# Kernel optimization log

Hardware: AMD Instinct MI355X
Metric: run time of the kernel (lower is better)

## Reference

```python
import math
import jax, jax.numpy as jnp
import numpy as np

N = 2048
HID = 1024
ALPHA = 0.5
BETA = 0.1  # greedy term is zero when coords is None


def setup_inputs() -> dict:
    key = jax.random.key(0)
    k1, k2, k3, k4 = jax.random.split(key, 4)
    node_emb = jax.random.normal(k1, (N, HID), jnp.float32)
    demands = jax.random.uniform(k2, (N,), jnp.float32)  # each < 1 << capacity
    # query_net: Linear(hid+2 -> hid); key_net: Linear(hid -> hid)
    Wq = jax.random.normal(k3, (HID, HID + 2), jnp.float32) / math.sqrt(HID + 2)
    bq = jnp.zeros((HID,), jnp.float32)
    Wk = jax.random.normal(k4, (HID, HID), jnp.float32) / math.sqrt(HID)
    bk = jnp.zeros((HID,), jnp.float32)
    return {"node_emb": node_emb, "demands": demands, "Wq": Wq, "bq": bq,
            "Wk": Wk, "bk": bk, "capacity": 40, "depot_idx": 0}


def _decode(node_emb, demands, Wq, bq, Wk, bk, capacity, depot_idx):
    n, h = node_emb.shape
    cap = jnp.float32(capacity)
    inv_sqrt = 1.0 / math.sqrt(h)
    # key_net is a per-node linear map: precompute once (same math as per-step gather+linear)
    K = node_emb @ Wk.T + bk  # [N, H]
    idx = jnp.arange(n)
    # demands < 1, capacity = 40 => >= 39 customers per route => few depot returns;
    # T = N + N//8 safely bounds customer picks + route-closing depot emissions.
    T = n + n // 8
    visited0 = jnp.zeros((n,), bool).at[depot_idx].set(True)

    def step(carry, _):
        visited, load, last, done = carry
        feasible = (~visited) & (demands <= load)
        has_cand = jnp.any(feasible)
        # context = [emb(last), load/capacity, avgd]; avgd = 0 since coords is None
        ctx = jnp.concatenate([node_emb[last],
                               jnp.stack([load / cap, jnp.float32(0.0)])])
        q = Wq @ ctx + bq                      # [H]
        s = ALPHA * ((K @ q) * inv_sqrt)       # [N] scores over all nodes
        s_m = jnp.where(feasible, s, -jnp.inf)
        cand = jnp.argmax(s_m)
        take = has_cand & (~done)
        nxt = jnp.where(take, cand, depot_idx).astype(jnp.int32)
        step_score = jnp.where(take, s[cand], jnp.float32(0.0))
        visited = visited | ((idx == cand) & take)
        load = jnp.where(take, load - demands[cand], cap)  # route end resets load
        done = done | ((~take) & jnp.all(visited))
        return (visited, load, nxt, done), (nxt, step_score)

    carry0 = (visited0, cap, jnp.int32(depot_idx), jnp.bool_(False))
    _, (seq, scores) = jax.lax.scan(step, carry0, None, length=T)
    tour = jnp.concatenate([jnp.array([depot_idx], seq.dtype), seq])  # [T+1]
    return tour, scores


def reference(node_emb, demands, Wq, bq, Wk, bk, capacity, depot_idx):
    # tour: flat visitation order; routes are the segments between depot occurrences
    # (trailing depots are padding once all customers are served).
    # scores: selected decoder score at each step (0 at depot/padding steps).
    return _decode(node_emb, demands, Wq, bq, Wk, bk, capacity, depot_idx)
```

## Files before the change

### kernel.cpp

```cpp
#include <hip/hip_runtime.h>
#include <hip/hip_bf16.h>


#define NN 2048
#define HH 1024
#define TSTEPS (NN + NN / 8)
#define TILE 64
#define KT 16
#define KCAND 128
#define KL 15

__global__ __launch_bounds__(256) void prep_wqh(const float* __restrict__ Wq,
                                                float* __restrict__ Wqh) {
  int id = blockIdx.x * 256 + threadIdx.x;
  int r = id >> 10, c = id & 1023;
  Wqh[id] = Wq[r * (HH + 2) + c];
}

__global__ __launch_bounds__(256) void gemm_nt(const float* __restrict__ A, int lda,
                                               const float* __restrict__ B, int ldb,
                                               float* __restrict__ C, int ldc,
                                               int K, const float* __restrict__ bias) {
  __shared__ float As[KT][TILE + 4];
  __shared__ float Bs[KT][TILE + 4];
  const int i0 = blockIdx.y * TILE;
  const int j0 = blockIdx.x * TILE;
  const int t = threadIdx.x;
  const int srow = t >> 2, sq = t & 3;
  const int tx = t & 15, ty = t >> 4;
  float acc[4][4] = {};
  for (int k0 = 0; k0 < K; k0 += KT) {
    float4 av = *(const float4*)&A[(size_t)(i0 + srow) * lda + k0 + sq * 4];
    float4 bv = *(const float4*)&B[(size_t)(j0 + srow) * ldb + k0 + sq * 4];
    __syncthreads();
    As[sq * 4 + 0][srow] = av.x; As[sq * 4 + 1][srow] = av.y;
    As[sq * 4 + 2][srow] = av.z; As[sq * 4 + 3][srow] = av.w;
    Bs[sq * 4 + 0][srow] = bv.x; Bs[sq * 4 + 1][srow] = bv.y;
    Bs[sq * 4 + 2][srow] = bv.z; Bs[sq * 4 + 3][srow] = bv.w;
    __syncthreads();
#pragma unroll
    for (int k = 0; k < KT; ++k) {
      float4 a4 = *(const float4*)&As[k][ty * 4];
      float4 b4 = *(const float4*)&Bs[k][tx * 4];
      float a[4] = {a4.x, a4.y, a4.z, a4.w};
      float b[4] = {b4.x, b4.y, b4.z, b4.w};
#pragma unroll
      for (int m = 0; m < 4; ++m)
#pragma unroll
        for (int n = 0; n < 4; ++n) acc[m][n] = fmaf(a[m], b[n], acc[m][n]);
    }
  }
  float bb[4] = {0.f, 0.f, 0.f, 0.f};
  if (bias) {
#pragma unroll
    for (int n = 0; n < 4; ++n) bb[n] = bias[j0 + tx * 4 + n];
  }
#pragma unroll
  for (int m = 0; m < 4; ++m) {
    float4 st = {acc[m][0] + bb[0], acc[m][1] + bb[1], acc[m][2] + bb[2], acc[m][3] + bb[3]};
    *(float4*)&C[(size_t)(i0 + ty * 4 + m) * ldc + j0 + tx * 4] = st;
  }
}

__global__ __launch_bounds__(64) void uv_k(const float* __restrict__ Kmat,
                                           const float* __restrict__ Wq,
                                           const float* __restrict__ bq,
                                           float* __restrict__ u, float* __restrict__ v) {
  int i = blockIdx.x;
  int lane = threadIdx.x;
  float su = 0.f, sv = 0.f;
#pragma unroll
  for (int m = 0; m < HH / 64; ++m) {
    int j = lane + 64 * m;
    float kv = Kmat[(size_t)i * HH + j];
    su = fmaf(kv, Wq[(size_t)j * (HH + 2) + HH], su);
    sv = fmaf(kv, bq[j], sv);
  }
#pragma unroll
  for (int off = 32; off; off >>= 1) {
    su += __shfl_down(su, off, 64);
    sv += __shfl_down(sv, off, 64);
  }
  if (lane == 0) { u[i] = su; v[i] = sv; }
}

__global__ __launch_bounds__(256) void umax_k(const float* __restrict__ u,
                                              float* __restrict__ umaxp) {
  __shared__ float sm[256];
  int t = threadIdx.x;
  float m = 0.f;
  for (int i = t; i < NN; i += 256) m = fmaxf(m, fabsf(u[i]));
  sm[t] = m;
  __syncthreads();
  for (int s = 128; s; s >>= 1) {
    if (t < s) sm[t] = fmaxf(sm[t], sm[t + s]);
    __syncthreads();
  }
  if (t == 0) *umaxp = sm[0];
}

__device__ __forceinline__ unsigned f2key(float f) {
  unsigned x = __float_as_uint(f);
  return x ^ ((x >> 31) ? 0xFFFFFFFFu : 0x80000000u);
}
__device__ __forceinline__ float key2f(unsigned k) {
  unsigned x = (k & 0x80000000u) ? (k ^ 0x80000000u) : ~k;
  return __uint_as_float(x);
}
__device__ __forceinline__ unsigned ub16(float x) {
  unsigned b = __float_as_uint(x);
  if (x > 0.f && (b & 0xFFFFu)) b += 0x10000u;
  return b >> 16;
}
__global__ __launch_bounds__(256) void prep_cand(const float* __restrict__ GT,
                                                 uint2* __restrict__ cand,
                                                 unsigned* __restrict__ pc16,
                                                 unsigned* __restrict__ thrpk) {
  __shared__ float rowv[NN];
  __shared__ int hist[256];
  __shared__ unsigned c128k[KCAND];
  __shared__ int c128i[KCAND];
  __shared__ int s_d, s_need, s_gt, s_eq, s_gt2, s_eq2, s_flag;
  const int row = blockIdx.x, t = threadIdx.x;
  for (int i = t; i < NN; i += 256) rowv[i] = GT[(size_t)row * NN + i];
  __syncthreads();
  unsigned prefix = 0;
  int need = KCAND;
  for (int pass = 0; pass < 4; ++pass) {
    hist[t] = 0;
    __syncthreads();
    const int shift = 24 - 8 * pass;
    for (int i = t; i < NN; i += 256) {
      unsigned k = f2key(rowv[i]);
      if (pass == 0 || (k >> (shift + 8)) == (prefix >> (shift + 8)))
        atomicAdd(&hist[(k >> shift) & 0xFF], 1);
    }
    __syncthreads();
    if (t == 0) {
      int cum = 0, d = 255;
      for (; d > 0; --d) {
        if (cum + hist[d] >= need) break;
        cum += hist[d];
      }
      s_d = d;
      s_need = need - cum;
    }
    __syncthreads();
    prefix |= ((unsigned)s_d) << shift;
    need = s_need;
    __syncthreads();
  }
  const unsigned thrk = prefix;
  if (t == 0) { s_gt = 0; s_eq = 0; }
  __syncthreads();
  for (int i = t; i < NN; i += 256) {
    unsigned k = f2key(rowv[i]);
    if (k > thrk) {
      int p = atomicAdd(&s_gt, 1);
      cand[(size_t)row * KCAND + p] = make_uint2(__float_as_uint(rowv[i]), (unsigned)i);
      c128k[p] = k;
      c128i[p] = i;
    }
  }
  __syncthreads();
  const int cgt = s_gt;
  for (int i = t; i < NN; i += 256) {
    if (f2key(rowv[i]) == thrk) {
      int p = atomicAdd(&s_eq, 1);
      if (p < KCAND - cgt) {
        cand[(size_t)row * KCAND + cgt + p] = make_uint2(__float_as_uint(rowv[i]), (unsigned)i);
        c128k[cgt + p] = thrk;
        c128i[cgt + p] = i;
      }
    }
  }
  __syncthreads();
  unsigned pfx2 = 0;
  need = KL;
  for (int pass = 0; pass < 4; ++pass) {
    hist[t] = 0;
    __syncthreads();
    const int shift = 24 - 8 * pass;
    for (int i = t; i < KCAND; i += 256) {
      unsigned k = c128k[i];
      if (pass == 0 || (k >> (shift + 8)) == (pfx2 >> (shift + 8)))
        atomicAdd(&hist[(k >> shift) & 0xFF], 1);
    }
    __syncthreads();
    if (t == 0) {
      int cum = 0, d = 255;
      for (; d > 0; --d) {
        if (cum + hist[d] >= need) break;
        cum += hist[d];
      }
      s_d = d;
      s_need = need - cum;
    }
    __syncthreads();
    pfx2 |= ((unsigned)s_d) << shift;
    need = s_need;
    __syncthreads();
  }
  const unsigned thrk15 = pfx2;
  if (t == 0) { s_gt2 = 0; s_eq2 = 0; s_flag = 0; }
  __syncthreads();
  for (int i = t; i < KCAND; i += 256) {
    if (c128k[i] > thrk15) {
      int p = atomicAdd(&s_gt2, 1);
      pc16[(size_t)row * KL + p] = (c128k[i] & 0xFFFFF800u) | (unsigned)c128i[i];
      if (fabsf(key2f(c128k[i])) >= 128.0f) s_flag = 1;
    }
  }
  __syncthreads();
  const int cgt2 = s_gt2;
  for (int i = t; i < KCAND; i += 256) {
    if (c128k[i] == thrk15) {
      int p = atomicAdd(&s_eq2, 1);
      if (p < KL - cgt2)
        pc16[(size_t)row * KL + cgt2 + p] = (thrk15 & 0xFFFFF800u) | (unsigned)c128i[i];
    }
  }
  if (t == 0 && fabsf(key2f(thrk15)) >= 128.0f) s_flag = 1;
  __syncthreads();
  if (t == 0) {
    float t15 = s_flag ? __builtin_inff() : key2f(thrk15);
    thrpk[row] = (ub16(t15) << 16) | ub16(key2f(thrk));
  }
}

__global__ __launch_bounds__(256) void warm_k(const float* __restrict__ a, int n,
                                              float* __restrict__ sink) {
  float s = 0.f;
  const float4* a4 = (const float4*)a;
  for (int i = threadIdx.x; i < n / 4; i += 256) {
    float4 x = a4[i];
    s += x.x + x.y + x.z + x.w;
  }
  if (s == 1.2345e-30f) sink[blockIdx.x] = s;
}

#define DPP_MERGE2(CTRL)                                                      \
  {                                                                           \
    int ovb = __builtin_amdgcn_update_dpp(                                    \
        (int)0xFF800000, __float_as_int(bv), (CTRL), 0xf, 0xf, false);        \
    int oib = __builtin_amdgcn_update_dpp(                                    \
        0x7fffffff, bi, (CTRL), 0xf, 0xf, false);                             \
    float ov = __int_as_float(ovb);                                           \
    if (ov > bv || (ov == bv && oib < bi)) { bv = ov; bi = oib; }             \
  }

#define DPP_TOP2(CTRL)                                                        \
  {                                                                           \
    int ovb = __builtin_amdgcn_update_dpp(                                    \
        (int)0xFF800000, __float_as_int(bv1), (CTRL), 0xf, 0xf, false);       \
    int oib = __builtin_amdgcn_update_dpp(                                    \
        0x7fffffff, bi1, (CTRL), 0xf, 0xf, false);                            \
    int ov2b = __builtin_amdgcn_update_dpp(                                   \
        (int)0xFF800000, __float_as_int(bv2), (CTRL), 0xf, 0xf, false);       \
    float ov1 = __int_as_float(ovb);                                          \
    float ov2 = __int_as_float(ov2b);                                         \
    float lose = fminf(bv1, ov1);                                             \
    if (ov1 > bv1 || (ov1 == bv1 && oib < bi1)) { bv1 = ov1; bi1 = oib; }     \
    bv2 = fmaxf(fmaxf(bv2, ov2), lose);                                       \
  }

__global__ __launch_bounds__(64, 1) void decode(const float* __restrict__ GT,
                                                const uint2* __restrict__ cand,
                                                const unsigned* __restrict__ pc16,
                                                const unsigned* __restrict__ thrpkg,
                                                const float* __restrict__ umaxp,
                                                const float* __restrict__ u,
                                                const float* __restrict__ demands,
                                                const int* __restrict__ capp,
                                                const int* __restrict__ depotp,
                                                float* __restrict__ out) {
  __shared__ __align__(16) unsigned s_pc[NN * KL + 64];
  __shared__ __align__(16) float2 s_du[NN];
  __shared__ __align__(16) unsigned s_thr[NN];
  __shared__ __align__(16) float s_lr[TSTEPS];
  __shared__ __align__(16) unsigned short s_tour[TSTEPS + 2];

  const int lane = threadIdx.x;
  const int depot = *depotp;
  const float capf = (float)(*capp);
  const float umaxv = *umaxp;
  const float INF = __builtin_inff();
  const float NEGINF = -INF;
  const float C0 = 0.015625f;
  const float MARGIN = 0.5f;
  const float EGM = 0.0625f;
  float* sduf = (float*)s_du;

  for (int i = lane; i < NN; i += 64) {
    s_du[i] = make_float2(demands[i], u[i]);
    s_thr[i] = thrpkg[i];
  }
  {
    const uint4* p4 = (const uint4*)pc16;
    uint4* q4 = (uint4*)s_pc;
    for (int i = lane; i < NN * KL / 4; i += 64) q4[i] = p4[i];
  }
  if (lane == 0) {
    sduf[2 * depot] = INF;
    s_tour[0] = (unsigned short)depot;
  }

  int done = 0, ntaken = 0, lasts = depot;
  float load = capf;
  float lr = load / capf;
  int step = 0;
  const int lcl = (lane < KL) ? lane : (KL - 1);

  for (; step < TSTEPS; ++step) {
    const int row = lasts;
    unsigned pw = s_pc[row * KL + lcl];
    unsigned pk = s_thr[row];
    int i1x = (int)(pw & 0x7FFu);
    float g1 = key2f(pw & 0xFFFFF800u);
    float2 du1 = s_du[i1x];
    float t1 = fmaf(du1.y, lr, g1);
    bool act = (lane < KL) && (du1.x <= load);
    float bv1 = act ? t1 : NEGINF;
    int bi1 = act ? i1x : 0x7fffffff;
    float bv2 = NEGINF;
    DPP_TOP2(0x111); DPP_TOP2(0x112); DPP_TOP2(0x114); DPP_TOP2(0x118);
    float rv1 = __int_as_float(__builtin_amdgcn_readlane(__float_as_int(bv1), 15));
    int ri1 = __builtin_amdgcn_readlane(bi1, 15);
    float rv2 = __int_as_float(__builtin_amdgcn_readlane(__float_as_int(bv2), 15));
    float thr1 = __uint_as_float(pk & 0xFFFF0000u);
    const float B1 = fmaf(lr, umaxv, thr1) + MARGIN;
    int take, nxt;
    if (rv1 > B1 && rv1 > rv2 + EGM) {
      take = 1; nxt = ri1;
    } else {
      uint4 cc = ((const uint4*)(cand + (size_t)row * KCAND))[lane];
      float bv = NEGINF;
      int bi = 0x7fffffff;
      {
        float ga = __uint_as_float(cc.x); int ia = (int)cc.y;
        float gb = __uint_as_float(cc.z); int ib = (int)cc.w;
        float2 da = s_du[ia];
        float2 db = s_du[ib];
        float ta = fmaf(da.y, lr, ga);
        float tb = fmaf(db.y, lr, gb);
        if ((da.x <= load) && (ta > bv || (ta == bv && ia < bi))) { bv = ta; bi = ia; }
        if ((db.x <= load) && (tb > bv || (tb == bv && ib < bi))) { bv = tb; bi = ib; }
      }
      DPP_MERGE2(0x111); DPP_MERGE2(0x112); DPP_MERGE2(0x114);
      DPP_MERGE2(0x118); DPP_MERGE2(0x142); DPP_MERGE2(0x143);
      float rbv = __int_as_float(__builtin_amdgcn_readlane(__float_as_int(bv), 63));
      int rbi = __builtin_amdgcn_readlane(bi, 63);
      float thr2 = __uint_as_float(pk << 16);
      const float B2 = fmaf(lr, umaxv, thr2) + MARGIN;
      if (rbv > B2) {
        take = 1; nxt = rbi;
      } else {
        const float4* rowp = (const float4*)(GT + (size_t)row * NN);
        const float4* du4 = (const float4*)s_du;
        float fv = NEGINF;
        int fi = NN;
#pragma unroll
        for (int r = 0; r < 8; ++r) {
          float4 g4 = rowp[r * 64 + lane];
          float4 pA = du4[(r * 64 + lane) * 2];
          float4 pB = du4[(r * 64 + lane) * 2 + 1];
          float gl[4] = {g4.x, g4.y, g4.z, g4.w};
          float dl[4] = {pA.x, pA.z, pB.x, pB.z};
          float ul[4] = {pA.y, pA.w, pB.y, pB.w};
          float cv = NEGINF;
          int cj = 0;
#pragma unroll
          for (int j = 0; j < 4; ++j) {
            float tt = fmaf(ul[j], lr, gl[j]);
            bool feas = (dl[j] <= load);
            if (feas && tt > cv) { cv = tt; cj = j; }
          }
          if (cv > fv) { fv = cv; fi = 4 * (r * 64 + lane) + cj; }
        }
        float bv = fv;
        int bi = fi;
        DPP_MERGE2(0x111); DPP_MERGE2(0x112); DPP_MERGE2(0x114);
        DPP_MERGE2(0x118); DPP_MERGE2(0x142); DPP_MERGE2(0x143);
        float fbv = __int_as_float(__builtin_amdgcn_readlane(__float_as_int(bv), 63));
        int fbi = __builtin_amdgcn_readlane(bi, 63);
        take = (fbv > NEGINF) ? 1 : 0;
        nxt = take ? fbi : depot;
      }
    }

    if (lane == 0) {
      s_tour[1 + step] = (unsigned short)nxt;
      s_lr[step] = take ? lr : -1.0f;
    }
    if (take) {
      float dwin = s_du[nxt].x;
      load = load - dwin;
      ntaken++;
      if (lane == 0) sduf[2 * nxt] = INF;
    } else {
      load = capf;
      if (ntaken == NN - 1) done = 1;
    }
    lasts = nxt;
    lr = load / capf;
    if (done) { ++step; break; }
  }

  for (int q = step + lane; q < TSTEPS; q += 64) {
    s_tour[1 + q] = (unsigned short)depot;
    s_lr[q] = -1.0f;
  }
  for (int i = lane; i <= TSTEPS; i += 64) out[i] = (float)s_tour[i];
  for (int s = lane; s < TSTEPS; s += 64) {
    float lrs = s_lr[s];
    float sc = 0.0f;
    if (lrs >= 0.0f) {
      int lastI = (int)s_tour[s];
      int biI = (int)s_tour[s + 1];
      float g = GT[(size_t)lastI * NN + biI];
      sc = fmaf(s_du[biI].y, lrs, g) * C0;
    }
    out[1 + TSTEPS + s] = sc;
  }
}

extern "C" void kernel_launch(void* const* d_in, const int* in_sizes, int n_in,
                              void* d_out, int out_size, void* d_ws, size_t ws_size,
                              hipStream_t stream) {
  const float* emb     = (const float*)d_in[0];
  const float* demands = (const float*)d_in[1];
  const float* Wq      = (const float*)d_in[2];
  const float* bq      = (const float*)d_in[3];
  const float* Wk      = (const float*)d_in[4];
  const float* bk      = (const float*)d_in[5];
  const int* cap       = (const int*)d_in[6];
  const int* depot     = (const int*)d_in[7];
  float* out           = (float*)d_out;

  char* ws = (char*)d_ws;
  float* Kmat = (float*)(ws);
  float* Z    = (float*)(ws + ((size_t)8 << 20));
  float* GT   = (float*)(ws + ((size_t)16 << 20));
  float* Wqh  = (float*)(ws + ((size_t)32 << 20));
  float* u    = (float*)(ws + ((size_t)36 << 20));
  float* v    = (float*)(ws + ((size_t)36 << 20) + 8192);
  unsigned* thrpkg = (unsigned*)(ws + ((size_t)36 << 20) + 16384);
  float* umax = (float*)(ws + ((size_t)36 << 20) + 24576);
  float* sink = (float*)(ws + ((size_t)36 << 20) + 32768);
  uint2* cnd  = (uint2*)Wqh;
  unsigned* pc16g = (unsigned*)(ws + ((size_t)34 << 20));

  hipLaunchKernelGGL(prep_wqh, dim3(4096), dim3(256), 0, stream, Wq, Wqh);
  hipLaunchKernelGGL(gemm_nt, dim3(HH / TILE, NN / TILE), dim3(256), 0, stream,
                     emb, HH, Wk, HH, Kmat, HH, HH, bk);
  hipLaunchKernelGGL(gemm_nt, dim3(HH / TILE, NN / TILE), dim3(256), 0, stream,
                     emb, HH, Wqh, HH, Z, HH, HH, (const float*)nullptr);
  hipLaunchKernelGGL(uv_k, dim3(NN), dim3(64), 0, stream, Kmat, Wq, bq, u, v);
  hipLaunchKernelGGL(umax_k, dim3(1), dim3(256), 0, stream, u, umax);
  hipLaunchKernelGGL(gemm_nt, dim3(NN / TILE, NN / TILE), dim3(256), 0, stream,
                     Z, HH, Kmat, HH, GT, NN, HH, v);
  hipLaunchKernelGGL(prep_cand, dim3(NN), dim3(256), 0, stream, GT, cnd,
                     pc16g, thrpkg);
  hipLaunchKernelGGL(warm_k, dim3(128), dim3(256), 0, stream,
                     (const float*)cnd, NN * KCAND * 2, sink);
  hipLaunchKernelGGL(decode, dim3(1), dim3(64), 0, stream, GT, cnd,
                     pc16g, thrpkg, umax, u, demands, cap, depot, out);
}
```

Measured before the change: 1.905 ms.

## Tighten per-row candidate pruning bounds using excluded-set maxima of G+u

Replaces the global |u| max bound with per-row bounds built from the max of G+u over nodes outside the top-15 and top-128 sets, interpolated by load ratio. The goal is for the cheap top-15 and top-128 tiers to certify the argmax more often, so the sequential decode loop falls back to full-row scans less frequently. It also packs score and index into one key for a cheaper DPP top-2 reduction, moves the full-row scan into a noinline function to lighten the hot loop, and moves the per-step lr log from LDS to global memory. In exchange, prep_cand does an extra pass per row and needs more shared memory.

```diff
diff --git a/kernel.cpp b/kernel.cpp
--- a/kernel.cpp
+++ b/kernel.cpp
@@ -84,21 +84,6 @@
   if (lane == 0) { u[i] = su; v[i] = sv; }
 }
 
-__global__ __launch_bounds__(256) void umax_k(const float* __restrict__ u,
-                                              float* __restrict__ umaxp) {
-  __shared__ float sm[256];
-  int t = threadIdx.x;
-  float m = 0.f;
-  for (int i = t; i < NN; i += 256) m = fmaxf(m, fabsf(u[i]));
-  sm[t] = m;
-  __syncthreads();
-  for (int s = 128; s; s >>= 1) {
-    if (t < s) sm[t] = fmaxf(sm[t], sm[t + s]);
-    __syncthreads();
-  }
-  if (t == 0) *umaxp = sm[0];
-}
-
 __device__ __forceinline__ unsigned f2key(float f) {
   unsigned x = __float_as_uint(f);
   return x ^ ((x >> 31) ? 0xFFFFFFFFu : 0x80000000u);
@@ -113,16 +98,27 @@
   return b >> 16;
 }
 __global__ __launch_bounds__(256) void prep_cand(const float* __restrict__ GT,
+                                                 const float* __restrict__ u,
                                                  uint2* __restrict__ cand,
                                                  unsigned* __restrict__ pc16,
-                                                 unsigned* __restrict__ thrpk) {
+                                                 uint2* __restrict__ thrpk2) {
   __shared__ float rowv[NN];
+  __shared__ float su_[NN];
   __shared__ int hist[256];
+  __shared__ float red15[256];
+  __shared__ float red128[256];
   __shared__ unsigned c128k[KCAND];
   __shared__ int c128i[KCAND];
+  __shared__ unsigned char markA[NN];
+  __shared__ unsigned char markB[NN];
   __shared__ int s_d, s_need, s_gt, s_eq, s_gt2, s_eq2, s_flag;
   const int row = blockIdx.x, t = threadIdx.x;
-  for (int i = t; i < NN; i += 256) rowv[i] = GT[(size_t)row * NN + i];
+  for (int i = t; i < NN; i += 256) {
+    rowv[i] = GT[(size_t)row * NN + i];
+    su_[i] = u[i];
+    markA[i] = 0;
+    markB[i] = 0;
+  }
   __syncthreads();
   unsigned prefix = 0;
   int need = KCAND;
@@ -160,6 +156,7 @@
       cand[(size_t)row * KCAND + p] = make_uint2(__float_as_uint(rowv[i]), (unsigned)i);
       c128k[p] = k;
       c128i[p] = i;
+      markA[i] = 1;
     }
   }
   __syncthreads();
@@ -171,6 +168,7 @@
         cand[(size_t)row * KCAND + cgt + p] = make_uint2(__float_as_uint(rowv[i]), (unsigned)i);
         c128k[cgt + p] = thrk;
         c128i[cgt + p] = i;
+        markA[i] = 1;
       }
     }
   }
@@ -208,7 +206,8 @@
     if (c128k[i] > thrk15) {
       int p = atomicAdd(&s_gt2, 1);
       pc16[(size_t)row * KL + p] = (c128k[i] & 0xFFFFF800u) | (unsigned)c128i[i];
-      if (fabsf(key2f(c128k[i])) >= 128.0f) s_flag = 1;
+      markB[c128i[i]] = 1;
+      if (fabsf(key2f(c128k[i])) + fabsf(su_[c128i[i]]) >= 128.0f) s_flag = 1;
     }
   }
   __syncthreads();
@@ -216,15 +215,37 @@
   for (int i = t; i < KCAND; i += 256) {
     if (c128k[i] == thrk15) {
       int p = atomicAdd(&s_eq2, 1);
-      if (p < KL - cgt2)
+      if (p < KL - cgt2) {
         pc16[(size_t)row * KL + cgt2 + p] = (thrk15 & 0xFFFFF800u) | (unsigned)c128i[i];
+        markB[c128i[i]] = 1;
+        if (fabsf(key2f(thrk15)) + fabsf(su_[c128i[i]]) >= 128.0f) s_flag = 1;
+      }
     }
   }
   if (t == 0 && fabsf(key2f(thrk15)) >= 128.0f) s_flag = 1;
   __syncthreads();
+  float lm15 = -__builtin_inff(), lm128 = -__builtin_inff();
+  for (int i = t; i < NN; i += 256) {
+    float gu = rowv[i] + su_[i];
+    if (!markB[i]) lm15 = fmaxf(lm15, gu);
+    if (!markA[i]) lm128 = fmaxf(lm128, gu);
+  }
+  red15[t] = lm15;
+  red128[t] = lm128;
+  __syncthreads();
+  for (int s = 128; s; s >>= 1) {
+    if (t < s) {
+      red15[t] = fmaxf(red15[t], red15[t + s]);
+      red128[t] = fmaxf(red128[t], red128[t + s]);
+    }
+    __syncthreads();
+  }
   if (t == 0) {
-    float t15 = s_flag ? __builtin_inff() : key2f(thrk15);
-    thrpk[row] = (ub16(t15) << 16) | ub16(key2f(thrk));
+    const float INF = __builtin_inff();
+    float t15 = s_flag ? INF : key2f(thrk15);
+    float m15 = s_flag ? INF : red15[0];
+    thrpk2[row] = make_uint2((ub16(t15) << 16) | ub16(m15),
+                             (ub16(key2f(thrk)) << 16) | ub16(red128[0]));
   }
 }
 
@@ -249,43 +270,76 @@
     if (ov > bv || (ov == bv && oib < bi)) { bv = ov; bi = oib; }             \
   }
 
-#define DPP_TOP2(CTRL)                                                        \
+#define KRED(CTRL)                                                            \
   {                                                                           \
-    int ovb = __builtin_amdgcn_update_dpp(                                    \
-        (int)0xFF800000, __float_as_int(bv1), (CTRL), 0xf, 0xf, false);       \
-    int oib = __builtin_amdgcn_update_dpp(                                    \
-        0x7fffffff, bi1, (CTRL), 0xf, 0xf, false);                            \
-    int ov2b = __builtin_amdgcn_update_dpp(                                   \
-        (int)0xFF800000, __float_as_int(bv2), (CTRL), 0xf, 0xf, false);       \
-    float ov1 = __int_as_float(ovb);                                          \
-    float ov2 = __int_as_float(ov2b);                                         \
-    float lose = fminf(bv1, ov1);                                             \
-    if (ov1 > bv1 || (ov1 == bv1 && oib < bi1)) { bv1 = ov1; bi1 = oib; }     \
-    bv2 = fmaxf(fmaxf(bv2, ov2), lose);                                       \
-  }
+    unsigned o1 = (unsigned)__builtin_amdgcn_update_dpp(                      \
+        0, (int)m1, (CTRL), 0xf, 0xf, false);                                 \
+    unsigned o2 = (unsigned)__builtin_amdgcn_update_dpp(                      \
+        0, (int)m2, (CTRL), 0xf, 0xf, false);                                 \
+    unsigned mn = min(m1, o1);                                                \
+    m1 = max(m1, o1);                                                         \
+    m2 = max(max(m2, o2), mn);                                                \
+  }
+
+struct Pick { int take; int nxt; };
+
+__device__ __noinline__ Pick tier3_scan(const float* __restrict__ GT,
+                                        const float2* sdu, int row, int lane,
+                                        float load, float lr, int depot) {
+  const float NEGINF = -__builtin_inff();
+  const float4* rowp = (const float4*)(GT + (size_t)row * NN);
+  const float4* du4 = (const float4*)sdu;
+  float fv = NEGINF;
+  int fi = NN;
+#pragma unroll
+  for (int r = 0; r < 8; ++r) {
+    float4 g4 = rowp[r * 64 + lane];
+    float4 pA = du4[(r * 64 + lane) * 2];
+    float4 pB = du4[(r * 64 + lane) * 2 + 1];
+    float gl[4] = {g4.x, g4.y, g4.z, g4.w};
+    float dl[4] = {pA.x, pA.z, pB.x, pB.z};
+    float ul[4] = {pA.y, pA.w, pB.y, pB.w};
+    float cv = NEGINF;
+    int cj = 0;
+#pragma unroll
+    for (int j = 0; j < 4; ++j) {
+      float tt = fmaf(ul[j], lr, gl[j]);
+      bool feas = (dl[j] <= load);
+      if (feas && tt > cv) { cv = tt; cj = j; }
+    }
+    if (cv > fv) { fv = cv; fi = 4 * (r * 64 + lane) + cj; }
+  }
+  float bv = fv;
+  int bi = fi;
+  DPP_MERGE2(0x111); DPP_MERGE2(0x112); DPP_MERGE2(0x114);
+  DPP_MERGE2(0x118); DPP_MERGE2(0x142); DPP_MERGE2(0x143);
+  float fbv = __int_as_float(__builtin_amdgcn_readlane(__float_as_int(bv), 63));
+  int fbi = __builtin_amdgcn_readlane(bi, 63);
+  Pick p;
+  p.take = (fbv > NEGINF) ? 1 : 0;
+  p.nxt = p.take ? fbi : depot;
+  return p;
+}
 
 __global__ __launch_bounds__(64, 1) void decode(const float* __restrict__ GT,
                                                 const uint2* __restrict__ cand,
                                                 const unsigned* __restrict__ pc16,
-                                                const unsigned* __restrict__ thrpkg,
-                                                const float* __restrict__ umaxp,
+                                                const uint2* __restrict__ thrpk2,
                                                 const float* __restrict__ u,
                                                 const float* __restrict__ demands,
                                                 const int* __restrict__ capp,
                                                 const int* __restrict__ depotp,
+                                                float* __restrict__ lrbuf,
                                                 float* __restrict__ out) {
   __shared__ __align__(16) unsigned s_pc[NN * KL + 64];
   __shared__ __align__(16) float2 s_du[NN];
-  __shared__ __align__(16) unsigned s_thr[NN];
-  __shared__ __align__(16) float s_lr[TSTEPS];
+  __shared__ __align__(16) uint2 s_thr[NN];
   __shared__ __align__(16) unsigned short s_tour[TSTEPS + 2];
 
   const int lane = threadIdx.x;
   const int depot = *depotp;
   const float capf = (float)(*capp);
-  const float umaxv = *umaxp;
   const float INF = __builtin_inff();
-  const float NEGINF = -INF;
   const float C0 = 0.015625f;
   const float MARGIN = 0.5f;
   const float EGM = 0.0625f;
@@ -293,7 +347,7 @@
 
   for (int i = lane; i < NN; i += 64) {
     s_du[i] = make_float2(demands[i], u[i]);
-    s_thr[i] = thrpkg[i];
+    s_thr[i] = thrpk2[i];
   }
   {
     const uint4* p4 = (const uint4*)pc16;
@@ -305,7 +359,7 @@
     s_tour[0] = (unsigned short)depot;
   }
 
-  int done = 0, ntaken = 0, lasts = depot;
+  int ntaken = 0, lasts = depot;
   float load = capf;
   float lr = load / capf;
   int step = 0;
@@ -314,27 +368,29 @@
   for (; step < TSTEPS; ++step) {
     const int row = lasts;
     unsigned pw = s_pc[row * KL + lcl];
-    unsigned pk = s_thr[row];
+    uint2 pk2 = s_thr[row];
     int i1x = (int)(pw & 0x7FFu);
+    float2 du1 = s_du[i1x];
     float g1 = key2f(pw & 0xFFFFF800u);
-    float2 du1 = s_du[i1x];
     float t1 = fmaf(du1.y, lr, g1);
     bool act = (lane < KL) && (du1.x <= load);
-    float bv1 = act ? t1 : NEGINF;
-    int bi1 = act ? i1x : 0x7fffffff;
-    float bv2 = NEGINF;
-    DPP_TOP2(0x111); DPP_TOP2(0x112); DPP_TOP2(0x114); DPP_TOP2(0x118);
-    float rv1 = __int_as_float(__builtin_amdgcn_readlane(__float_as_int(bv1), 15));
-    int ri1 = __builtin_amdgcn_readlane(bi1, 15);
-    float rv2 = __int_as_float(__builtin_amdgcn_readlane(__float_as_int(bv2), 15));
-    float thr1 = __uint_as_float(pk & 0xFFFF0000u);
-    const float B1 = fmaf(lr, umaxv, thr1) + MARGIN;
+    unsigned m1 = act ? ((f2key(t1) & 0xFFFFF800u) | ((~(unsigned)i1x) & 0x7FFu)) : 0u;
+    unsigned m2 = 0u;
+    KRED(0x111); KRED(0x112); KRED(0x114); KRED(0x118);
+    unsigned rv1k = (unsigned)__builtin_amdgcn_readlane((int)m1, 15);
+    unsigned rv2k = (unsigned)__builtin_amdgcn_readlane((int)m2, 15);
+    float rv1f = key2f(rv1k & 0xFFFFF800u);
+    float rv2f = key2f(rv2k | 0x7FFu);
+    float t15 = __uint_as_float(pk2.x & 0xFFFF0000u);
+    float m15 = __uint_as_float(pk2.x << 16);
+    float B1 = fmaf(1.0f - lr, t15, lr * m15) + MARGIN;
     int take, nxt;
-    if (rv1 > B1 && rv1 > rv2 + EGM) {
-      take = 1; nxt = ri1;
+    if (__builtin_expect((rv1f > B1) && (rv1f > rv2f + EGM), 1)) {
+      take = 1;
+      nxt = (int)((~rv1k) & 0x7FFu);
     } else {
       uint4 cc = ((const uint4*)(cand + (size_t)row * KCAND))[lane];
-      float bv = NEGINF;
+      float bv = -INF;
       int bi = 0x7fffffff;
       {
         float ga = __uint_as_float(cc.x); int ia = (int)cc.y;
@@ -350,47 +406,20 @@
       DPP_MERGE2(0x118); DPP_MERGE2(0x142); DPP_MERGE2(0x143);
       float rbv = __int_as_float(__builtin_amdgcn_readlane(__float_as_int(bv), 63));
       int rbi = __builtin_amdgcn_readlane(bi, 63);
-      float thr2 = __uint_as_float(pk << 16);
-      const float B2 = fmaf(lr, umaxv, thr2) + MARGIN;
+      float t128 = __uint_as_float(pk2.y & 0xFFFF0000u);
+      float m128 = __uint_as_float(pk2.y << 16);
+      float B2 = fmaf(1.0f - lr, t128, lr * m128) + MARGIN;
       if (rbv > B2) {
         take = 1; nxt = rbi;
       } else {
-        const float4* rowp = (const float4*)(GT + (size_t)row * NN);
-        const float4* du4 = (const float4*)s_du;
-        float fv = NEGINF;
-        int fi = NN;
-#pragma unroll
-        for (int r = 0; r < 8; ++r) {
-          float4 g4 = rowp[r * 64 + lane];
-          float4 pA = du4[(r * 64 + lane) * 2];
-          float4 pB = du4[(r * 64 + lane) * 2 + 1];
-          float gl[4] = {g4.x, g4.y, g4.z, g4.w};
-          float dl[4] = {pA.x, pA.z, pB.x, pB.z};
-          float ul[4] = {pA.y, pA.w, pB.y, pB.w};
-          float cv = NEGINF;
-          int cj = 0;
-#pragma unroll
-          for (int j = 0; j < 4; ++j) {
-            float tt = fmaf(ul[j], lr, gl[j]);
-            bool feas = (dl[j] <= load);
-            if (feas && tt > cv) { cv = tt; cj = j; }
-          }
-          if (cv > fv) { fv = cv; fi = 4 * (r * 64 + lane) + cj; }
-        }
-        float bv = fv;
-        int bi = fi;
-        DPP_MERGE2(0x111); DPP_MERGE2(0x112); DPP_MERGE2(0x114);
-        DPP_MERGE2(0x118); DPP_MERGE2(0x142); DPP_MERGE2(0x143);
-        float fbv = __int_as_float(__builtin_amdgcn_readlane(__float_as_int(bv), 63));
-        int fbi = __builtin_amdgcn_readlane(bi, 63);
-        take = (fbv > NEGINF) ? 1 : 0;
-        nxt = take ? fbi : depot;
+        Pick p = tier3_scan(GT, (const float2*)s_du, row, lane, load, lr, depot);
+        take = p.take; nxt = p.nxt;
       }
     }
 
     if (lane == 0) {
       s_tour[1 + step] = (unsigned short)nxt;
-      s_lr[step] = take ? lr : -1.0f;
+      lrbuf[step] = take ? lr : -1.0f;
     }
     if (take) {
       float dwin = s_du[nxt].x;
@@ -399,20 +428,20 @@
       if (lane == 0) sduf[2 * nxt] = INF;
     } else {
       load = capf;
-      if (ntaken == NN - 1) done = 1;
+      if (ntaken == NN - 1) { ++step; break; }
     }
     lasts = nxt;
     lr = load / capf;
-    if (done) { ++step; break; }
   }
 
   for (int q = step + lane; q < TSTEPS; q += 64) {
     s_tour[1 + q] = (unsigned short)depot;
-    s_lr[q] = -1.0f;
-  }
+    lrbuf[q] = -1.0f;
+  }
+  asm volatile("s_waitcnt vmcnt(0)" ::: "memory");
   for (int i = lane; i <= TSTEPS; i += 64) out[i] = (float)s_tour[i];
   for (int s = lane; s < TSTEPS; s += 64) {
-    float lrs = s_lr[s];
+    float lrs = lrbuf[s];
     float sc = 0.0f;
     if (lrs >= 0.0f) {
       int lastI = (int)s_tour[s];
@@ -444,11 +473,11 @@
   float* Wqh  = (float*)(ws + ((size_t)32 << 20));
   float* u    = (float*)(ws + ((size_t)36 << 20));
   float* v    = (float*)(ws + ((size_t)36 << 20) + 8192);
-  unsigned* thrpkg = (unsigned*)(ws + ((size_t)36 << 20) + 16384);
-  float* umax = (float*)(ws + ((size_t)36 << 20) + 24576);
   float* sink = (float*)(ws + ((size_t)36 << 20) + 32768);
   uint2* cnd  = (uint2*)Wqh;
   unsigned* pc16g = (unsigned*)(ws + ((size_t)34 << 20));
+  uint2* thrpk2g  = (uint2*)(ws + ((size_t)34 << 20) + (128 << 10));
+  float* lrbuf    = (float*)(ws + ((size_t)34 << 20) + (160 << 10));
 
   hipLaunchKernelGGL(prep_wqh, dim3(4096), dim3(256), 0, stream, Wq, Wqh);
   hipLaunchKernelGGL(gemm_nt, dim3(HH / TILE, NN / TILE), dim3(256), 0, stream,
@@ -456,13 +485,12 @@
   hipLaunchKernelGGL(gemm_nt, dim3(HH / TILE, NN / TILE), dim3(256), 0, stream,
                      emb, HH, Wqh, HH, Z, HH, HH, (const float*)nullptr);
   hipLaunchKernelGGL(uv_k, dim3(NN), dim3(64), 0, stream, Kmat, Wq, bq, u, v);
-  hipLaunchKernelGGL(umax_k, dim3(1), dim3(256), 0, stream, u, umax);
   hipLaunchKernelGGL(gemm_nt, dim3(NN / TILE, NN / TILE), dim3(256), 0, stream,
                      Z, HH, Kmat, HH, GT, NN, HH, v);
-  hipLaunchKernelGGL(prep_cand, dim3(NN), dim3(256), 0, stream, GT, cnd,
-                     pc16g, thrpkg);
+  hipLaunchKernelGGL(prep_cand, dim3(NN), dim3(256), 0, stream, GT, u, cnd,
+                     pc16g, thrpk2g);
   hipLaunchKernelGGL(warm_k, dim3(128), dim3(256), 0, stream,
-                     (const float*)cnd, NN * KCAND * 2, sink);
+                     (const float*)cnd, NN * KCAND * 2 + (160 << 8), sink);
   hipLaunchKernelGGL(decode, dim3(1), dim3(64), 0, stream, GT, cnd,
-                     pc16g, thrpkg, umax, u, demands, cap, depot, out);
-}
+                     pc16g, thrpk2g, u, demands, cap, depot, lrbuf, out);
+}
```

New measurement: 1.837 ms. 3.6% less time.
